# Performance work log

Measured on AMD Instinct MI355X. Metric: run time of the kernel, lower is better.

Reference implementation:

```python
import jax, jax.numpy as jnp
import numpy as np

T_DEC = 60  # decoder steps, hard-coded in the original forward

def _conv1d(x, w, b):
    # x: [B, C_in, L], w: [C_out, C_in, K] -> [B, C_out, L-K+1] (valid conv)
    y = jax.lax.conv_general_dilated(x, w, window_strides=(1,), padding='VALID',
                                     dimension_numbers=('NCH', 'OIH', 'NCH'))
    return y + b[None, :, None]

def _lstm_cell(x, h, c, wih, whh, bih, bhh):
    # PyTorch LSTM cell, gate order i, f, g, o
    g = x @ wih.T + h @ whh.T + (bih + bhh)
    i, f, gg, o = jnp.split(g, 4, axis=-1)
    c = jax.nn.sigmoid(f) * c + jax.nn.sigmoid(i) * jnp.tanh(gg)
    h = jax.nn.sigmoid(o) * jnp.tanh(c)
    return h, c

def _lstm_seq(xs, wih, whh, bih, bhh, reverse=False):
    # xs: [B, T, D] -> [B, T, H], zero initial state (PyTorch default)
    B, H = xs.shape[0], whh.shape[1]
    xs_t = jnp.swapaxes(xs, 0, 1)
    if reverse:
        xs_t = xs_t[::-1]
    def step(carry, x):
        h, c = carry
        h, c = _lstm_cell(x, h, c, wih, whh, bih, bhh)
        return (h, c), h
    init = (jnp.zeros((B, H), xs.dtype), jnp.zeros((B, H), xs.dtype))
    _, hs = jax.lax.scan(step, init, xs_t)
    if reverse:
        hs = hs[::-1]
    return jnp.swapaxes(hs, 0, 1)

def setup_inputs():
    key = jax.random.key(0)
    B, L, D_in, H, D_out = 64, 4096, 64, 256, 128
    C1, C2, C3 = 8, 16, 32
    ks = jax.random.split(key, 32)
    it = iter(ks)
    def p(shape, scale=0.1):
        return jax.random.normal(next(it), shape, jnp.float32) * scale
    inp = {}
    inp['x'] = jax.random.normal(next(it), (B, L, D_in), jnp.float32)
    inp['conv_w1'] = p((C1, D_in, 4)); inp['conv_b1'] = p((C1,))
    inp['conv_w2'] = p((C2, C1, 8));  inp['conv_b2'] = p((C2,))
    inp['conv_w3'] = p((C3, C2, 16)); inp['conv_b3'] = p((C3,))
    inp['attn_w'] = p((H, C3)); inp['attn_b'] = p((H,))
    inp['dec1_wih'] = p((2, 4 * H, C3)); inp['dec1_whh'] = p((2, 4 * H, H))
    inp['dec1_bih'] = p((2, 4 * H));     inp['dec1_bhh'] = p((2, 4 * H))
    inp['dec2_wih0'] = p((2, 4 * H, 2 * H)); inp['dec2_whh0'] = p((2, 4 * H, H))
    inp['dec2_bih0'] = p((2, 4 * H));        inp['dec2_bhh0'] = p((2, 4 * H))
    inp['dec2_wih1'] = p((2, 4 * H, 2 * H)); inp['dec2_whh1'] = p((2, 4 * H, H))
    inp['dec2_bih1'] = p((2, 4 * H));        inp['dec2_bhh1'] = p((2, 4 * H))
    inp['out_w'] = p((D_out, 2 * H)); inp['out_b'] = p((D_out,))
    return inp

def reference(x, conv_w1, conv_b1, conv_w2, conv_b2, conv_w3, conv_b3,
              attn_w, attn_b, dec1_wih, dec1_whh, dec1_bih, dec1_bhh,
              dec2_wih0, dec2_whh0, dec2_bih0, dec2_bhh0,
              dec2_wih1, dec2_whh1, dec2_bih1, dec2_bhh1, out_w, out_b):
    # Eval mode: all dropouts are identity.
    h = jnp.swapaxes(x, 1, 2)  # [B, D_in, L]
    h = jax.nn.relu(_conv1d(h, conv_w1, conv_b1))
    h = jax.nn.relu(_conv1d(h, conv_w2, conv_b2))
    h = jax.nn.relu(_conv1d(h, conv_w3, conv_b3))
    enc = jnp.swapaxes(h, 1, 2)  # [B, Lp, 32], Lp = L - 25
    keys_t = jnp.einsum('blc,hc->bhl', enc, attn_w) + attn_b[None, :, None]  # [B, H, Lp]
    B, H = x.shape[0], attn_w.shape[0]

    def dec1(wih, whh, bih, bhh):
        def step(carry, _):
            hh, cc = carry
            align = jnp.einsum('bh,bhl->bl', hh, keys_t)   # attention scores over Lp
            a = jax.nn.softmax(align, axis=-1)
            ctx = jnp.einsum('bl,blc->bc', a, enc)         # context [B, 32]
            hh, cc = _lstm_cell(ctx, hh, cc, wih, whh, bih, bhh)
            return (hh, cc), hh
        init = (jnp.zeros((B, H), x.dtype), jnp.zeros((B, H), x.dtype))
        _, hs = jax.lax.scan(step, init, None, length=T_DEC)
        return jnp.swapaxes(hs, 0, 1)  # [B, 60, H]

    fwd = dec1(dec1_wih[0], dec1_whh[0], dec1_bih[0], dec1_bhh[0])
    # the bkwd branch writes step i into slot 60-i-1, i.e. time-reversed outputs
    bkwd = dec1(dec1_wih[1], dec1_whh[1], dec1_bih[1], dec1_bhh[1])[:, ::-1]
    d2in = jnp.concatenate([fwd, bkwd], axis=-1)  # [B, 60, 2H]
    l0 = jnp.concatenate([
        _lstm_seq(d2in, dec2_wih0[0], dec2_whh0[0], dec2_bih0[0], dec2_bhh0[0]),
        _lstm_seq(d2in, dec2_wih0[1], dec2_whh0[1], dec2_bih0[1], dec2_bhh0[1], reverse=True)], axis=-1)
    l1 = jnp.concatenate([
        _lstm_seq(l0, dec2_wih1[0], dec2_whh1[0], dec2_bih1[0], dec2_bhh1[0]),
        _lstm_seq(l0, dec2_wih1[1], dec2_whh1[1], dec2_bih1[1], dec2_bhh1[1], reverse=True)], axis=-1)
    return l1 @ out_w.T + out_b  # [B, 60, D_out]
```

## Files before the change

### kernel.cpp

```cpp
#include <hip/hip_runtime.h>

#define B_    64
#define L1C   4093
#define L2C   4086
#define L3C   4071
#define TDEC  60

static __device__ __forceinline__ float sigf(float x){ return 1.f/(1.f + __expf(-x)); }

typedef _Float16 h2_t __attribute__((ext_vector_type(2)));
union U2H { unsigned u; h2_t h; };

static __device__ __forceinline__ unsigned pkh2(float a, float b){
  U2H r; r.h[0] = (_Float16)a; r.h[1] = (_Float16)b; return r.u;
}
static __device__ __forceinline__ float dot2f(unsigned w, unsigned h, float acc){
  U2H a; a.u = w; U2H b; b.u = h;
#if __has_builtin(__builtin_amdgcn_fdot2)
  return __builtin_amdgcn_fdot2(a.h, b.h, acc, false);
#else
  acc = fmaf((float)a.h[0], (float)b.h[0], acc);
  acc = fmaf((float)a.h[1], (float)b.h[1], acc);
  return acc;
#endif
}

#define DOT8(g, wv, hv) \
  g = dot2f(wv.x, hv.x, g); g = dot2f(wv.y, hv.y, g); \
  g = dot2f(wv.z, hv.z, g); g = dot2f(wv.w, hv.w, g);

template<int CTRL>
static __device__ __forceinline__ float dppadd(float x){
  int y = __builtin_amdgcn_update_dpp(0, __float_as_int(x), CTRL, 0xf, 0xf, true);
  return x + __int_as_float(y);
}

template<int CIN,int COUT,int KW,int CINP>
__global__ __launch_bounds__(256) void k_convL(
    const float* __restrict__ in, const float* __restrict__ w,
    const float* __restrict__ bias, float* __restrict__ outp,
    int Lin_, int Lout_)
{
  __shared__ float xs[(256+KW-1)*CINP];
  int bi = blockIdx.y, l0 = blockIdx.x*256, tid = threadIdx.x;
  int nrow = min(256+KW-1, Lin_-l0);
  const float* ip = in + ((size_t)bi*Lin_ + l0)*CIN;
  for (int i = tid; i < nrow*(CIN/4); i += 256){
    int rr = i/(CIN/4), cc = i - rr*(CIN/4);
    float4 v = *(const float4*)(ip + rr*CIN + cc*4);
    float* dst = &xs[rr*CINP + cc*4];
    dst[0]=v.x; dst[1]=v.y; dst[2]=v.z; dst[3]=v.w;
  }
  __syncthreads();
  int l = l0 + tid;
  if (l >= Lout_) return;
  float acc[COUT];
#pragma unroll
  for (int o=0;o<COUT;o++) acc[o] = bias[o];
  for (int k=0;k<KW;k++){
    const float* xr = &xs[(tid+k)*CINP];
#pragma unroll
    for (int i=0;i<CIN;i++){
      float xv = xr[i];
#pragma unroll
      for (int o=0;o<COUT;o++)
        acc[o] = fmaf(xv, w[(o*CIN + i)*KW + k], acc[o]);
    }
  }
  float* op = outp + ((size_t)bi*Lout_ + l)*COUT;
#pragma unroll
  for (int o=0;o<COUT;o++) op[o] = fmaxf(acc[o], 0.f);
}

__global__ __launch_bounds__(256) void k_conv3qL(
    const float* __restrict__ in, const float* __restrict__ w,
    const float* __restrict__ bias, uint4* __restrict__ encq,
    float* __restrict__ encs, int Lin_, int Lout_)
{
  __shared__ float xs[(256+15)*17];
  int bi = blockIdx.y, l0 = blockIdx.x*256, tid = threadIdx.x;
  int nrow = min(256+15, Lin_-l0);
  const float* ip = in + ((size_t)bi*Lin_ + l0)*16;
  for (int i = tid; i < nrow*4; i += 256){
    int rr = i>>2, cc = i&3;
    float4 v = *(const float4*)(ip + rr*16 + cc*4);
    float* dst = &xs[rr*17 + cc*4];
    dst[0]=v.x; dst[1]=v.y; dst[2]=v.z; dst[3]=v.w;
  }
  __syncthreads();
  int l = l0 + tid;
  if (l >= Lout_) return;
  float acc[32];
#pragma unroll
  for (int o=0;o<32;o++) acc[o] = bias[o];
  for (int k=0;k<16;k++){
    const float* xr = &xs[(tid+k)*17];
#pragma unroll
    for (int i=0;i<16;i++){
      float xv = xr[i];
#pragma unroll
      for (int o=0;o<32;o++)
        acc[o] = fmaf(xv, w[(o*16 + i)*16 + k], acc[o]);
    }
  }
  float mx = 0.f;
#pragma unroll
  for (int o=0;o<32;o++){ acc[o] = fmaxf(acc[o],0.f); mx = fmaxf(mx, acc[o]); }
  float scale = mx * (1.f/255.f);
  float inv = (mx > 0.f) ? (255.f/mx) : 0.f;
  unsigned qs[8];
#pragma unroll
  for (int q8=0;q8<8;q8++){
    unsigned q0 = (unsigned)(acc[q8*4+0]*inv + 0.5f);
    unsigned q1 = (unsigned)(acc[q8*4+1]*inv + 0.5f);
    unsigned q2 = (unsigned)(acc[q8*4+2]*inv + 0.5f);
    unsigned q3 = (unsigned)(acc[q8*4+3]*inv + 0.5f);
    qs[q8] = q0 | (q1<<8) | (q2<<16) | (q3<<24);
  }
  uint4* op = encq + ((size_t)bi*Lout_ + l)*2;
  op[0] = make_uint4(qs[0],qs[1],qs[2],qs[3]);
  op[1] = make_uint4(qs[4],qs[5],qs[6],qs[7]);
  encs[(size_t)bi*Lout_ + l] = scale;
}

__global__ __launch_bounds__(256) void k_packwh(
    const float* __restrict__ w, uint4* __restrict__ wT, int K)
{
  int gid = blockIdx.x*256 + threadIdx.x;
  int per = (K/8)*1024;
  int d = gid / per, rem = gid - d*per;
  int j8 = rem >> 10, row = rem & 1023;
  const float* src = w + ((size_t)d*1024 + row)*K + j8*8;
  float4 a = *(const float4*)src;
  float4 b = *(const float4*)(src+4);
  uint4 o;
  o.x = pkh2(a.x, a.y);
  o.y = pkh2(a.z, a.w);
  o.z = pkh2(b.x, b.y);
  o.w = pkh2(b.z, b.w);
  wT[gid] = o;
}

#define CVT8(r, qv) \
  r[0]=(float)( qv.x      & 255u); r[1]=(float)((qv.x>>8 ) & 255u); \
  r[2]=(float)((qv.x>>16) & 255u); r[3]=(float)((qv.x>>24)       ); \
  r[4]=(float)( qv.y      & 255u); r[5]=(float)((qv.y>>8 ) & 255u); \
  r[6]=(float)((qv.y>>16) & 255u); r[7]=(float)((qv.y>>24)       );

__global__ __launch_bounds__(1024) void k_dec1g(
    const uint4* __restrict__ encq,
    const float* __restrict__ encs,
    const float* __restrict__ attn_w,
    const uint4* __restrict__ wihT,
    const uint4* __restrict__ whhT,
    const float* __restrict__ bih, const float* __restrict__ bhh,
    float* __restrict__ d2in)
{
  int b = blockIdx.x, d = blockIdx.y, tid = threadIdx.x;
  int c = tid & 3, rb = tid >> 2;

  __shared__ __align__(16) uint2 encQ2[16384];
  __shared__ float sls[4096];
  __shared__ __align__(16) float hls[256];
  __shared__ __align__(16) unsigned h2pk[128];
  __shared__ __align__(16) unsigned ctxh[16];
  __shared__ float vl[32];
  __shared__ float maxenc[32];
  __shared__ float Msh;
  __shared__ float red[1024];
  __shared__ float scr[512];
  __shared__ float gls[1024];

  {
    const uint4* src = encq + (size_t)b*L3C*2;
    uint4* dst = (uint4*)encQ2;
    for (int i = tid; i < 8192; i += 1024)
      dst[i] = (i < L3C*2) ? src[i] : make_uint4(0,0,0,0);
    const float* ss = encs + (size_t)b*L3C;
    for (int i = tid; i < 4096; i += 1024)
      sls[i] = (i < L3C) ? ss[i] : 0.f;
  }
  if (tid < 256) hls[tid] = 0.f;
  if (tid < 128) h2pk[tid] = 0u;
  float creg = 0.f;
  float bsum = bih[(size_t)d*1024 + tid] + bhh[(size_t)d*1024 + tid];
  const uint4* whp = whhT + (size_t)d*32768;
  __syncthreads();

  {
    float mc[8];
#pragma unroll
    for (int j=0;j<8;j++) mc[j] = 0.f;
#pragma unroll
    for (int k=0;k<16;k++){
      int l = rb + 256*k;
      uint2 qv = encQ2[l*4 + c];
      float sl = sls[l];
      float r[8]; CVT8(r, qv)
#pragma unroll
      for (int j=0;j<8;j++) mc[j] = fmaxf(mc[j], r[j]*sl);
    }
#pragma unroll
    for (int off=4; off<=32; off<<=1){
#pragma unroll
      for (int j=0;j<8;j++) mc[j] = fmaxf(mc[j], __shfl_xor(mc[j], off));
    }
    int wid = tid >> 6;
    if ((tid&63) < 4){
#pragma unroll
      for (int j=0;j<8;j++) scr[wid*32 + c*8 + j] = mc[j];
    }
    __syncthreads();
    if (tid < 32){
      float mm = 0.f;
#pragma unroll
      for (int w=0;w<16;w++) mm = fmaxf(mm, scr[w*32 + tid]);
      maxenc[tid] = mm;
    }
    __syncthreads();
  }

  for (int t=0; t<TDEC; t++){
    {
      int cc = tid & 31, part = tid >> 5;
      const float* wp = attn_w + (size_t)(part*8)*32 + cc;
      float s = 0.f;
#pragma unroll
      for (int k=0;k<8;k++) s = fmaf(hls[part*8+k], wp[k*32], s);
      red[tid] = s;
    }
    __syncthreads();
    if (tid < 32){
      float v = 0.f;
#pragma unroll
      for (int q=0;q<32;q++) v += red[q*32 + tid];
      vl[tid] = v;
      float mt = maxenc[tid] * fmaxf(v, 0.f);
#pragma unroll
      for (int off=1; off<32; off<<=1) mt += __shfl_xor(mt, off);
      if (tid==0) Msh = mt;
    }
    __syncthreads();

    float vreg[8];
#pragma unroll
    for (int j=0;j<8;j++) vreg[j] = vl[c*8 + j];
    float M = Msh;
    float ssum = 0.f;
    float acc[8];
#pragma unroll
    for (int j=0;j<8;j++) acc[j] = 0.f;
    float g = bsum;
#pragma unroll 4
    for (int k=0;k<16;k++){
      uint4 wv0 = whp[(2*k  )*1024 + tid];
      uint4 wv1 = whp[(2*k+1)*1024 + tid];
      int l = rb + 256*k;
      uint2 qv = encQ2[l*4 + c];
      float sl = sls[l];
      float r[8]; CVT8(r, qv)
      float s = 0.f;
#pragma unroll
      for (int j=0;j<8;j++) s = fmaf(r[j], vreg[j], s);
      s = dppadd<0xB1>(s);
      s = dppadd<0x4E>(s);
      s *= sl;
      if (l >= L3C) s = -3.0e38f;
      float e = __expf(s - M);
      ssum += e;
      float em = e * sl;
#pragma unroll
      for (int j=0;j<8;j++) acc[j] = fmaf(em, r[j], acc[j]);
      uint4 hv0 = *(const uint4*)&h2pk[(2*k  )*4];
      uint4 hv1 = *(const uint4*)&h2pk[(2*k+1)*4];
      DOT8(g, wv0, hv0)
      DOT8(g, wv1, hv1)
    }
    ssum = dppadd<0x124>(ssum); ssum = dppadd<0x128>(ssum);
    ssum += __shfl_xor(ssum, 16); ssum += __shfl_xor(ssum, 32);
#pragma unroll
    for (int j=0;j<8;j++){
      acc[j] = dppadd<0x124>(acc[j]); acc[j] = dppadd<0x128>(acc[j]);
      acc[j] += __shfl_xor(acc[j], 16); acc[j] += __shfl_xor(acc[j], 32);
    }
    int wid = tid >> 6;
    if ((tid&63) < 4){
#pragma unroll
      for (int j=0;j<8;j++) scr[wid*32 + c*8 + j] = acc[j];
    }
    if ((tid&63)==0) red[wid] = ssum;
    __syncthreads();
    if (tid < 32){
      float S = 0.f, s2 = 0.f;
#pragma unroll
      for (int w=0;w<16;w++){ S += red[w]; s2 += scr[w*32 + tid]; }
      float cv = s2 / S;
      float co = __shfl_xor(cv, 1);
      if (!(tid&1)) ctxh[tid>>1] = pkh2(cv, co);
    }
    __syncthreads();

#pragma unroll
    for (int c8=0;c8<4;c8++){
      uint4 wv = wihT[(size_t)d*4096 + c8*1024 + tid];
      uint4 hv = *(const uint4*)&ctxh[c8*4];
      DOT8(g, wv, hv)
    }
    gls[tid] = g;
    __syncthreads();
    if (tid < 256){
      float ii = sigf(gls[tid]);
      float ff = sigf(gls[256+tid]);
      float gg = tanhf(gls[512+tid]);
      float oo = sigf(gls[768+tid]);
      creg = fmaf(ff, creg, ii*gg);
      float hn = oo * tanhf(creg);
      hls[tid] = hn;
      float ho = __shfl_xor(hn, 1);
      if (!(tid&1)) h2pk[tid>>1] = pkh2(hn, ho);
      int tout = d ? (59 - t) : t;
      d2in[((size_t)b*60 + tout)*512 + d*256 + tid] = hn;
    }
    __syncthreads();
  }
}

__global__ __launch_bounds__(256) void k_gemm(
    const float* __restrict__ A, const float* __restrict__ W,
    float* __restrict__ C, const float* __restrict__ b1, const float* __restrict__ b2,
    int K, int ldc, size_t sW, size_t sC, int sB)
{
  int m0 = blockIdx.x * 128, n0 = blockIdx.y * 128, z = blockIdx.z;
  const float* Wz = W + (size_t)z*sW;
  float* Cz = C + (size_t)z*sC;
  const float* b1z = b1 + (size_t)z*sB;
  const float* b2z = b2 ? (b2 + (size_t)z*sB) : nullptr;
  __shared__ __align__(16) float As[16][132];
  __shared__ __align__(16) float Bs[16][132];
  int tid = threadIdx.x;
  int tx = tid & 15, ty = tid >> 4;
  int r = tid >> 2, c4 = tid & 3;
  float acc[8][8] = {};
  for (int k0=0; k0<K; k0+=16){
#pragma unroll
    for (int h=0; h<2; h++){
      int rr = r + h*64;
      float4 av = *(const float4*)(A  + (size_t)(m0+rr)*K + k0 + c4*4);
      float4 bv = *(const float4*)(Wz + (size_t)(n0+rr)*K + k0 + c4*4);
      As[c4*4+0][rr]=av.x; As[c4*4+1][rr]=av.y; As[c4*4+2][rr]=av.z; As[c4*4+3][rr]=av.w;
      Bs[c4*4+0][rr]=bv.x; Bs[c4*4+1][rr]=bv.y; Bs[c4*4+2][rr]=bv.z; Bs[c4*4+3][rr]=bv.w;
    }
    __syncthreads();
#pragma unroll
    for (int kk=0; kk<16; kk++){
      float a[8], bb[8];
      *(float4*)&a[0]  = *(const float4*)&As[kk][ty*8];
      *(float4*)&a[4]  = *(const float4*)&As[kk][ty*8+4];
      *(float4*)&bb[0] = *(const float4*)&Bs[kk][tx*8];
      *(float4*)&bb[4] = *(const float4*)&Bs[kk][tx*8+4];
#pragma unroll
      for (int i=0;i<8;i++)
#pragma unroll
        for (int j=0;j<8;j++)
          acc[i][j] = fmaf(a[i], bb[j], acc[i][j]);
    }
    __syncthreads();
  }
  float bb1[8];
#pragma unroll
  for (int j=0;j<8;j++){
    int n = n0 + tx*8 + j;
    bb1[j] = b1z[n] + (b2z ? b2z[n] : 0.f);
  }
#pragma unroll
  for (int i=0;i<8;i++){
    int m = m0 + ty*8 + i;
    float o[8];
#pragma unroll
    for (int j=0;j<8;j++) o[j] = acc[i][j] + bb1[j];
    *(float4*)(Cz + (size_t)m*ldc + n0 + tx*8)     = *(const float4*)&o[0];
    *(float4*)(Cz + (size_t)m*ldc + n0 + tx*8 + 4) = *(const float4*)&o[4];
  }
}

__global__ __launch_bounds__(1024) void k_rec2(
    const float* __restrict__ xg,
    const uint4* __restrict__ wT,
    float* __restrict__ out)
{
  int b = blockIdx.x, d = blockIdx.y, tid = threadIdx.x;
  __shared__ __align__(16) unsigned h2pk[128];
  __shared__ float gls[1024];
  float c = 0.f;
  if (tid < 128) h2pk[tid] = 0u;
  const uint4* wp = wT + (size_t)d*32*1024;
  uint4 wpre[20];
#pragma unroll
  for (int j=0;j<20;j++) wpre[j] = wp[j*1024 + tid];
  const float* xp = xg + (((size_t)d*64 + b)*60)*1024;
  __syncthreads();
  for (int step=0; step<TDEC; step++){
    int t = d ? (TDEC-1-step) : step;
    float g = xp[(size_t)t*1024 + tid];
#pragma unroll
    for (int j8=0;j8<20;j8++){
      uint4 hv = *(const uint4*)&h2pk[j8*4];
      DOT8(g, wpre[j8], hv)
    }
#pragma unroll 4
    for (int j8=20;j8<32;j8++){
      uint4 wv = wp[j8*1024 + tid];
      uint4 hv = *(const uint4*)&h2pk[j8*4];
      DOT8(g, wv, hv)
    }
    gls[tid] = g;
    __syncthreads();
    if (tid < 256){
      float ii = sigf(gls[tid]);
      float ff = sigf(gls[256+tid]);
      float gg = tanhf(gls[512+tid]);
      float oo = sigf(gls[768+tid]);
      c = fmaf(ff, c, ii*gg);
      float hn = oo * tanhf(c);
      float ho = __shfl_xor(hn, 1);
      if (!(tid&1)) h2pk[tid>>1] = pkh2(hn, ho);
      out[((size_t)b*60 + t)*512 + d*256 + tid] = hn;
    }
    __syncthreads();
  }
}

extern "C" void kernel_launch(void* const* d_in, const int* in_sizes, int n_in,
                              void* d_out, int out_size, void* d_ws, size_t ws_size,
                              hipStream_t stream) {
  const float* x      = (const float*)d_in[0];
  const float* cw1    = (const float*)d_in[1];
  const float* cb1    = (const float*)d_in[2];
  const float* cw2    = (const float*)d_in[3];
  const float* cb2    = (const float*)d_in[4];
  const float* cw3    = (const float*)d_in[5];
  const float* cb3    = (const float*)d_in[6];
  const float* attn_w = (const float*)d_in[7];
  const float* d1_wih = (const float*)d_in[9];
  const float* d1_whh = (const float*)d_in[10];
  const float* d1_bih = (const float*)d_in[11];
  const float* d1_bhh = (const float*)d_in[12];
  const float* w2_ih0 = (const float*)d_in[13];
  const float* w2_hh0 = (const float*)d_in[14];
  const float* b2_ih0 = (const float*)d_in[15];
  const float* b2_hh0 = (const float*)d_in[16];
  const float* w2_ih1 = (const float*)d_in[17];
  const float* w2_hh1 = (const float*)d_in[18];
  const float* b2_ih1 = (const float*)d_in[19];
  const float* b2_hh1 = (const float*)d_in[20];
  const float* out_w  = (const float*)d_in[21];
  const float* out_b  = (const float*)d_in[22];

  char* ws = (char*)d_ws;
  size_t off = 0;
  uint4* encq = (uint4*)(ws + off);
  float* encs = (float*)(ws + off + 8338432);
  off += 16675840;
  size_t off_h1 = off;
  float* h1buf = (float*)(ws + off); off += 8382464;
  float* h2buf = (float*)(ws + off); off += 16736256;
  float* d2in  = (float*)(ws + off_h1);
  float* l0    = (float*)(ws + off_h1 + 7864320);
  float* l1    = (float*)(ws + off_h1 + 15728640);
  uint4* wT    = (uint4*)(ws + off_h1 + 23592960);
  float* xg    = (float*)(ws + off); off += 31457280;
  uint4* d1whhT = (uint4*)xg;
  uint4* d1wihT = (uint4*)((char*)xg + 1048576);
  (void)ws_size; (void)in_sizes; (void)n_in; (void)out_size;

  k_packwh<<<256,256,0,stream>>>(d1_whh, d1whhT, 256);
  k_packwh<<<32, 256,0,stream>>>(d1_wih, d1wihT, 32);

  k_convL<64,8,4,65><<<dim3(16,B_),256,0,stream>>>(x, cw1, cb1, h1buf, 4096, L1C);
  k_convL<8,16,8,9><<<dim3(16,B_),256,0,stream>>>(h1buf, cw2, cb2, h2buf, L1C, L2C);
  k_conv3qL<<<dim3(16,B_),256,0,stream>>>(h2buf, cw3, cb3, encq, encs, L2C, L3C);

  k_dec1g<<<dim3(64,2),1024,0,stream>>>(encq, encs, attn_w, d1wihT, d1whhT,
                                        d1_bih, d1_bhh, d2in);

  k_packwh<<<256,256,0,stream>>>(w2_hh0, wT, 256);
  k_gemm<<<dim3(30,8,2),256,0,stream>>>(d2in, w2_ih0, xg, b2_ih0, b2_hh0,
                                        512, 1024, (size_t)1024*512, (size_t)3840*1024, 1024);
  k_rec2<<<dim3(64,2),1024,0,stream>>>(xg, wT, l0);
  k_packwh<<<256,256,0,stream>>>(w2_hh1, wT, 256);
  k_gemm<<<dim3(30,8,2),256,0,stream>>>(l0, w2_ih1, xg, b2_ih1, b2_hh1,
                                        512, 1024, (size_t)1024*512, (size_t)3840*1024, 1024);
  k_rec2<<<dim3(64,2),1024,0,stream>>>(xg, wT, l1);
  k_gemm<<<dim3(30,1,1),256,0,stream>>>(l1, out_w, (float*)d_out, out_b, nullptr,
                                        512, 128, 0, 0, 0);
}
```

Before: 1.616 ms.

## Use packed fp16 dot2 GEMM for decoder input projections and prefetch recurrent weights

```diff
diff --git a/kernel.cpp b/kernel.cpp
--- a/kernel.cpp
+++ b/kernel.cpp
@@ -185,6 +185,9 @@
   float creg = 0.f;
   float bsum = bih[(size_t)d*1024 + tid] + bhh[(size_t)d*1024 + tid];
   const uint4* whp = whhT + (size_t)d*32768;
+  uint4 wpre[12];
+#pragma unroll
+  for (int j=0;j<12;j++) wpre[j] = whp[j*1024 + tid];
   __syncthreads();
 
   {
@@ -251,10 +254,10 @@
 #pragma unroll
     for (int j=0;j<8;j++) acc[j] = 0.f;
     float g = bsum;
-#pragma unroll 4
+#pragma unroll
     for (int k=0;k<16;k++){
-      uint4 wv0 = whp[(2*k  )*1024 + tid];
-      uint4 wv1 = whp[(2*k+1)*1024 + tid];
+      uint4 wv0 = (k<6) ? wpre[2*k]   : whp[(2*k  )*1024 + tid];
+      uint4 wv1 = (k<6) ? wpre[2*k+1] : whp[(2*k+1)*1024 + tid];
       int l = rb + 256*k;
       uint2 qv = encQ2[l*4 + c];
       float sl = sls[l];
@@ -363,6 +366,70 @@
 #pragma unroll
         for (int j=0;j<8;j++)
           acc[i][j] = fmaf(a[i], bb[j], acc[i][j]);
+    }
+    __syncthreads();
+  }
+  float bb1[8];
+#pragma unroll
+  for (int j=0;j<8;j++){
+    int n = n0 + tx*8 + j;
+    bb1[j] = b1z[n] + (b2z ? b2z[n] : 0.f);
+  }
+#pragma unroll
+  for (int i=0;i<8;i++){
+    int m = m0 + ty*8 + i;
+    float o[8];
+#pragma unroll
+    for (int j=0;j<8;j++) o[j] = acc[i][j] + bb1[j];
+    *(float4*)(Cz + (size_t)m*ldc + n0 + tx*8)     = *(const float4*)&o[0];
+    *(float4*)(Cz + (size_t)m*ldc + n0 + tx*8 + 4) = *(const float4*)&o[4];
+  }
+}
+
+__global__ __launch_bounds__(256) void k_gemmh(
+    const float* __restrict__ A, const uint4* __restrict__ WhT,
+    float* __restrict__ C, const float* __restrict__ b1, const float* __restrict__ b2,
+    int K, int ldc, size_t sW, size_t sC, int sB)
+{
+  int m0 = blockIdx.x * 128, n0 = blockIdx.y * 128, z = blockIdx.z;
+  const uint4* Wz = WhT + (size_t)z*sW;
+  float* Cz = C + (size_t)z*sC;
+  const float* b1z = b1 + (size_t)z*sB;
+  const float* b2z = b2 ? (b2 + (size_t)z*sB) : nullptr;
+  __shared__ __align__(16) unsigned Ash[8][132];
+  __shared__ __align__(16) unsigned Bsh[8][132];
+  int tid = threadIdx.x;
+  int tx = tid & 15, ty = tid >> 4;
+  int r = tid >> 2, c4 = tid & 3;
+  int nB = tid >> 1, hhB = tid & 1;
+  float acc[8][8] = {};
+  for (int k0=0; k0<K; k0+=16){
+#pragma unroll
+    for (int h=0; h<2; h++){
+      int rr = r + h*64;
+      float4 av = *(const float4*)(A + (size_t)(m0+rr)*K + k0 + c4*4);
+      Ash[c4*2  ][rr] = pkh2(av.x, av.y);
+      Ash[c4*2+1][rr] = pkh2(av.z, av.w);
+    }
+    {
+      uint4 wv = Wz[(size_t)(k0/8 + hhB)*1024 + n0 + nB];
+      Bsh[hhB*4+0][nB] = wv.x; Bsh[hhB*4+1][nB] = wv.y;
+      Bsh[hhB*4+2][nB] = wv.z; Bsh[hhB*4+3][nB] = wv.w;
+    }
+    __syncthreads();
+#pragma unroll
+    for (int kk2=0; kk2<8; kk2++){
+      uint4 au0 = *(const uint4*)&Ash[kk2][ty*8];
+      uint4 au1 = *(const uint4*)&Ash[kk2][ty*8+4];
+      uint4 bu0 = *(const uint4*)&Bsh[kk2][tx*8];
+      uint4 bu1 = *(const uint4*)&Bsh[kk2][tx*8+4];
+      unsigned au[8] = {au0.x,au0.y,au0.z,au0.w,au1.x,au1.y,au1.z,au1.w};
+      unsigned bu[8] = {bu0.x,bu0.y,bu0.z,bu0.w,bu1.x,bu1.y,bu1.z,bu1.w};
+#pragma unroll
+      for (int i=0;i<8;i++)
+#pragma unroll
+        for (int j=0;j<8;j++)
+          acc[i][j] = dot2f(au[i], bu[j], acc[i][j]);
     }
     __syncthreads();
   }
@@ -460,6 +527,10 @@
   size_t off = 0;
   uint4* encq = (uint4*)(ws + off);
   float* encs = (float*)(ws + off + 8338432);
+  uint4* wih0T = (uint4*)(ws + 0);
+  uint4* wih1T = (uint4*)(ws + 2097152);
+  uint4* whh0T = (uint4*)(ws + 4194304);
+  uint4* whh1T = (uint4*)(ws + 5242880);
   off += 16675840;
   size_t off_h1 = off;
   float* h1buf = (float*)(ws + off); off += 8382464;
@@ -467,7 +538,6 @@
   float* d2in  = (float*)(ws + off_h1);
   float* l0    = (float*)(ws + off_h1 + 7864320);
   float* l1    = (float*)(ws + off_h1 + 15728640);
-  uint4* wT    = (uint4*)(ws + off_h1 + 23592960);
   float* xg    = (float*)(ws + off); off += 31457280;
   uint4* d1whhT = (uint4*)xg;
   uint4* d1wihT = (uint4*)((char*)xg + 1048576);
@@ -483,14 +553,17 @@
   k_dec1g<<<dim3(64,2),1024,0,stream>>>(encq, encs, attn_w, d1wihT, d1whhT,
                                         d1_bih, d1_bhh, d2in);
 
-  k_packwh<<<256,256,0,stream>>>(w2_hh0, wT, 256);
-  k_gemm<<<dim3(30,8,2),256,0,stream>>>(d2in, w2_ih0, xg, b2_ih0, b2_hh0,
-                                        512, 1024, (size_t)1024*512, (size_t)3840*1024, 1024);
-  k_rec2<<<dim3(64,2),1024,0,stream>>>(xg, wT, l0);
-  k_packwh<<<256,256,0,stream>>>(w2_hh1, wT, 256);
-  k_gemm<<<dim3(30,8,2),256,0,stream>>>(l0, w2_ih1, xg, b2_ih1, b2_hh1,
-                                        512, 1024, (size_t)1024*512, (size_t)3840*1024, 1024);
-  k_rec2<<<dim3(64,2),1024,0,stream>>>(xg, wT, l1);
+  k_packwh<<<512,256,0,stream>>>(w2_ih0, wih0T, 512);
+  k_packwh<<<512,256,0,stream>>>(w2_ih1, wih1T, 512);
+  k_packwh<<<256,256,0,stream>>>(w2_hh0, whh0T, 256);
+  k_packwh<<<256,256,0,stream>>>(w2_hh1, whh1T, 256);
+
+  k_gemmh<<<dim3(30,8,2),256,0,stream>>>(d2in, wih0T, xg, b2_ih0, b2_hh0,
+                                         512, 1024, (size_t)64*1024, (size_t)3840*1024, 1024);
+  k_rec2<<<dim3(64,2),1024,0,stream>>>(xg, whh0T, l0);
+  k_gemmh<<<dim3(30,8,2),256,0,stream>>>(l0, wih1T, xg, b2_ih1, b2_hh1,
+                                         512, 1024, (size_t)64*1024, (size_t)3840*1024, 1024);
+  k_rec2<<<dim3(64,2),1024,0,stream>>>(xg, whh1T, l1);
   k_gemm<<<dim3(30,1,1),256,0,stream>>>(l1, out_w, (float*)d_out, out_b, nullptr,
                                         512, 128, 0, 0, 0);
 }
```

Measured after the change: 3.265 ms. 2.02x slower.
